# Optimization experiments

Measured on AMD Instinct MI355X. Metric: run time of the kernel, lower is better.

Reference implementation:

```python
import jax, jax.numpy as jnp
import numpy as np

B, L, D, H = 2, 1000, 288, 8
DIM = D // H          # 36 per-head dim
DFF = 2 * D           # 576 conv-FFN hidden
KS = L // 4           # 250 sampled keys per query
NQ = L // 4           # 250 selected (active) queries
EPS = 1e-5


def _layernorm(x, g, b):
    mu = x.mean(-1, keepdims=True)
    var = ((x - mu) ** 2).mean(-1, keepdims=True)
    return (x - mu) * jax.lax.rsqrt(var + EPS) * g + b


def _prob_attention(q, k, v, index_key):
    # q,k,v: [b,h,L,dim]; index_key: [L, KS]
    b, h, l, dim = q.shape
    # sample KS keys per query row (gather): [b,h,L,KS,dim]
    k_samp = jnp.take(k, index_key, axis=2)
    # sampled scores: [b,h,L,KS]
    scores_samp = jnp.einsum('bhld,bhlkd->bhlk', q, k_samp)
    # sparsity measure M(q) = max - mean(over full l_key, as in source)
    measure = scores_samp.max(-1) - scores_samp.sum(-1) / l
    # top-NQ active queries per (b,h): [b,h,NQ]
    idx_q = jax.lax.top_k(measure, NQ)[1]
    q_sel = jnp.take_along_axis(q, idx_q[..., None], axis=2)  # [b,h,NQ,dim]
    sim = jnp.einsum('bhqd,bhkd->bhqk', q_sel, k) * (1.0 / np.sqrt(dim))
    attn = jax.nn.softmax(sim, axis=-1)
    out_sel = jnp.einsum('bhqk,bhkd->bhqd', attn, v)          # [b,h,NQ,dim]
    # lazy queries get mean(V); scatter active outputs in
    out = jnp.broadcast_to(v.mean(axis=2, keepdims=True), v.shape)
    bi = jnp.arange(b)[:, None, None]
    hi = jnp.arange(h)[None, :, None]
    out = out.at[bi, hi, idx_q].set(out_sel)
    return out  # [b,h,L,dim]


def reference(x, index_key, Wq, bq, Wk, bk, Wv, bv, W1, b1, W2, b2,
              ln1_g, ln1_b, ln2_g, ln2_b):
    b, l, d = x.shape
    # QKV projections -> [b,h,L,dim]
    q = (x @ Wq.T + bq).reshape(b, l, H, DIM).transpose(0, 2, 1, 3)
    k = (x @ Wk.T + bk).reshape(b, l, H, DIM).transpose(0, 2, 1, 3)
    v = (x @ Wv.T + bv).reshape(b, l, H, DIM).transpose(0, 2, 1, 3)
    attn = _prob_attention(q, k, v, index_key)
    attn = attn.transpose(0, 2, 1, 3).reshape(b, l, d)
    # residual + LN1 (dropout is identity in eval)
    h1 = _layernorm(x + attn, ln1_g, ln1_b)
    # conv FFN (kernel_size=1 conv == per-position linear), exact GELU
    f = jax.nn.gelu(h1 @ W1.T + b1, approximate=False)   # [b,l,DFF]
    f = jax.nn.gelu(f @ W2.T + b2, approximate=False)    # [b,l,d]
    return _layernorm(f + h1, ln2_g, ln2_b)


def setup_inputs() -> dict:
    key = jax.random.key(0)
    ks = jax.random.split(key, 10)
    s = 0.05
    return {
        'x': jax.random.normal(ks[0], (B, L, D), jnp.float32),
        'index_key': jax.random.randint(ks[1], (L, KS), 0, L),
        'Wq': jax.random.normal(ks[2], (D, D), jnp.float32) * s,
        'bq': jnp.zeros((D,), jnp.float32),
        'Wk': jax.random.normal(ks[3], (D, D), jnp.float32) * s,
        'bk': jnp.zeros((D,), jnp.float32),
        'Wv': jax.random.normal(ks[4], (D, D), jnp.float32) * s,
        'bv': jnp.zeros((D,), jnp.float32),
        'W1': jax.random.normal(ks[5], (DFF, D), jnp.float32) * s,
        'b1': jnp.zeros((DFF,), jnp.float32),
        'W2': jax.random.normal(ks[6], (D, DFF), jnp.float32) * s,
        'b2': jnp.zeros((D,), jnp.float32),
        'ln1_g': jnp.ones((D,), jnp.float32),
        'ln1_b': jnp.zeros((D,), jnp.float32),
        'ln2_g': jnp.ones((D,), jnp.float32),
        'ln2_b': jnp.zeros((D,), jnp.float32),
    }
```

## Files before the change

kernel.cpp:

```cpp
#include <hip/hip_runtime.h>
#include <hip/hip_bf16.h>
#include <math.h>

#define B_ 2
#define L_ 1000
#define D_ 288
#define H_ 8
#define DIM_ 36
#define DFF_ 576
#define KS_ 250
#define NQ_ 250
#define BH_ (B_ * H_)
#define EPS_ 1e-5f
#define PSTRIDE_ 40

__device__ __forceinline__ float gelu_exact(float x) {
    return 0.5f * x * (1.0f + erff(x * 0.70710678118654752f));
}

__device__ __forceinline__ float dot4(float4 a, float4 b) {
    return a.x * b.x + a.y * b.y + a.z * b.z + a.w * b.w;
}

__global__ __launch_bounds__(256) void transpose_kernel(
    const float* __restrict__ src, float* __restrict__ dst,
    int Rr, int Cc, int ntx)
{
    __shared__ float tile[32][33];
    const int t = blockIdx.x;
    const int ty0 = (t / ntx) * 32, tx0 = (t % ntx) * 32;
    const int tx = threadIdx.x & 31, ty = threadIdx.x >> 5;
#pragma unroll
    for (int i = 0; i < 4; i++)
        tile[ty + 8 * i][tx] = src[(size_t)(ty0 + ty + 8 * i) * Cc + tx0 + tx];
    __syncthreads();
#pragma unroll
    for (int i = 0; i < 4; i++)
        dst[(size_t)(tx0 + ty + 8 * i) * Rr + ty0 + tx] = tile[tx][ty + 8 * i];
}

__global__ __launch_bounds__(256) void qkv_transpose_kernel(
    const float* __restrict__ Wq, const float* __restrict__ Wk,
    const float* __restrict__ Wv,
    float* __restrict__ WqT, float* __restrict__ WkT, float* __restrict__ WvT)
{
    __shared__ float tile[32][33];
    const int m = blockIdx.x / 81;
    const int t = blockIdx.x % 81;
    const float* src = (m == 0) ? Wq : (m == 1) ? Wk : Wv;
    float* dst = (m == 0) ? WqT : (m == 1) ? WkT : WvT;
    const int ty0 = (t / 9) * 32, tx0 = (t % 9) * 32;
    const int tx = threadIdx.x & 31, ty = threadIdx.x >> 5;
#pragma unroll
    for (int i = 0; i < 4; i++)
        tile[ty + 8 * i][tx] = src[(size_t)(ty0 + ty + 8 * i) * D_ + tx0 + tx];
    __syncthreads();
#pragma unroll
    for (int i = 0; i < 4; i++)
        dst[(size_t)(tx0 + ty + 8 * i) * D_ + ty0 + tx] = tile[tx][ty + 8 * i];
}

__global__ __launch_bounds__(256) void ktranspose_kernel(
    const float* __restrict__ K, float* __restrict__ KT)
{
    __shared__ float tile[32][33];
    const int t = blockIdx.x;
    const int bh = t >> 6;
    const int rem = t & 63;
    const int lt = rem >> 1, dt = rem & 1;
    const int l0 = lt * 32, d0 = dt * 32;
    const int tx = threadIdx.x & 31, ty = threadIdx.x >> 5;
    const float* Kb = K + (size_t)bh * L_ * DIM_;
    float* KTb = KT + (size_t)bh * DIM_ * L_;
#pragma unroll
    for (int i = 0; i < 4; i++) {
        int l = l0 + ty + 8 * i, d = d0 + tx;
        tile[ty + 8 * i][tx] = (l < L_ && d < DIM_) ? Kb[(size_t)l * DIM_ + d] : 0.f;
    }
    __syncthreads();
#pragma unroll
    for (int i = 0; i < 4; i++) {
        int d = d0 + ty + 8 * i, l = l0 + tx;
        if (d < DIM_ && l < L_) KTb[(size_t)d * L_ + l] = tile[tx][ty + 8 * i];
    }
}

__global__ __launch_bounds__(256) void qkvT2_kernel(
    const float* __restrict__ x,
    const float* __restrict__ WqT, const float* __restrict__ WkT,
    const float* __restrict__ WvT,
    const float* __restrict__ bq, const float* __restrict__ bk,
    const float* __restrict__ bv,
    float* __restrict__ Q, float* __restrict__ K, float* __restrict__ V)
{
    __shared__ float xsT[D_][4];
    const int base = blockIdx.x * 4;
    const int tid = threadIdx.x;

    for (int idx = tid; idx < 4 * D_; idx += 256) {
        int r = idx / D_, k = idx % D_;
        xsT[k][r] = x[(size_t)(base + r) * D_ + k];
    }
    __syncthreads();

    if (tid < 216) {
        const int gcol = 4 * tid;
        const int m = gcol / D_;
        const int c = gcol - m * D_;
        const float* WT = (m == 0) ? WqT : (m == 1) ? WkT : WvT;
        const float* bias = (m == 0) ? bq : (m == 1) ? bk : bv;
        float* outp = (m == 0) ? Q : (m == 1) ? K : V;

        float a[4][4];
#pragma unroll
        for (int j = 0; j < 4; j++) {
            float bv2 = bias[c + j];
#pragma unroll
            for (int r = 0; r < 4; r++) a[j][r] = bv2;
        }

        for (int k = 0; k < D_; k++) {
            float4 w = *(const float4*)(WT + (size_t)k * D_ + c);
            float4 xv = *(const float4*)&xsT[k][0];
            a[0][0] += w.x * xv.x; a[0][1] += w.x * xv.y; a[0][2] += w.x * xv.z; a[0][3] += w.x * xv.w;
            a[1][0] += w.y * xv.x; a[1][1] += w.y * xv.y; a[1][2] += w.y * xv.z; a[1][3] += w.y * xv.w;
            a[2][0] += w.z * xv.x; a[2][1] += w.z * xv.y; a[2][2] += w.z * xv.z; a[2][3] += w.z * xv.w;
            a[3][0] += w.w * xv.x; a[3][1] += w.w * xv.y; a[3][2] += w.w * xv.z; a[3][3] += w.w * xv.w;
        }

#pragma unroll
        for (int j = 0; j < 4; j++) {
            int col = c + j;
            int h = col / DIM_, dd = col % DIM_;
#pragma unroll
            for (int r = 0; r < 4; r++) {
                int row = base + r;
                int b = row / L_, l = row % L_;
                outp[((size_t)(b * H_ + h) * L_ + l) * DIM_ + dd] = a[j][r];
            }
        }
    }
}

__global__ __launch_bounds__(320) void qkv_kernel(
    const float* __restrict__ x,
    const float* __restrict__ Wq, const float* __restrict__ bq,
    const float* __restrict__ Wk, const float* __restrict__ bk,
    const float* __restrict__ Wv, const float* __restrict__ bv,
    float* __restrict__ Q, float* __restrict__ K, float* __restrict__ V)
{
    constexpr int R = 8;
    __shared__ float xs[R][D_];
    const int base = blockIdx.x * R;
    const int tid = threadIdx.x;

    const float4* xsrc = (const float4*)(x + (size_t)base * D_);
    float4* xdst = (float4*)&xs[0][0];
    for (int i = tid; i < R * D_ / 4; i += 320) xdst[i] = xsrc[i];
    __syncthreads();

    if (tid < D_) {
        const float4* wq4 = (const float4*)(Wq + (size_t)tid * D_);
        const float4* wk4 = (const float4*)(Wk + (size_t)tid * D_);
        const float4* wv4 = (const float4*)(Wv + (size_t)tid * D_);
        float aq[R], ak[R], av[R];
        float biasq = bq[tid], biask = bk[tid], biasv = bv[tid];
#pragma unroll
        for (int r = 0; r < R; r++) { aq[r] = biasq; ak[r] = biask; av[r] = biasv; }
        for (int d4 = 0; d4 < D_ / 4; d4++) {
            float4 wqv = wq4[d4], wkv = wk4[d4], wvv = wv4[d4];
#pragma unroll
            for (int r = 0; r < R; r++) {
                float4 hv = *(const float4*)&xs[r][d4 * 4];
                aq[r] += dot4(hv, wqv);
                ak[r] += dot4(hv, wkv);
                av[r] += dot4(hv, wvv);
            }
        }
        const int h = tid / DIM_, dd = tid % DIM_;
#pragma unroll
        for (int r = 0; r < R; r++) {
            int row = base + r;
            int b = row / L_, l = row % L_;
            size_t o = ((size_t)(b * H_ + h) * L_ + l) * DIM_ + dd;
            Q[o] = aq[r]; K[o] = ak[r]; V[o] = av[r];
        }
    }
}

__global__ __launch_bounds__(256) void vmean_kernel(
    const float* __restrict__ V, float* __restrict__ Vmean)
{
    const int bh = blockIdx.x;
    const int tid = threadIdx.x;
    __shared__ float red[7][DIM_];
    if (tid < 252) {
        int g = tid / DIM_, d = tid % DIM_;
        const float* base = V + (size_t)bh * L_ * DIM_;
        float s = 0.f;
        for (int l = g; l < L_; l += 7) s += base[l * DIM_ + d];
        red[g][d] = s;
    }
    __syncthreads();
    if (tid < DIM_) {
        float s = 0.f;
#pragma unroll
        for (int g = 0; g < 7; g++) s += red[g][tid];
        Vmean[bh * DIM_ + tid] = s * (1.0f / L_);
    }
}

__global__ __launch_bounds__(256) void score_measure3_kernel(
    const float* __restrict__ Q, const float* __restrict__ KT,
    const int* __restrict__ index_key, float* __restrict__ measure)
{
    constexpr int R = 8;
    __shared__ float qs[R][DIM_];
    __shared__ float st[R][1004];
    const int bh = blockIdx.x / 125;
    const int qt = blockIdx.x % 125;
    const int tid = threadIdx.x;

    if (tid < R * DIM_ / 4)
        ((float4*)&qs[0][0])[tid] =
            ((const float4*)(Q + ((size_t)bh * L_ + qt * R) * DIM_))[tid];
    __syncthreads();

    const float* KTb = KT + (size_t)bh * DIM_ * L_;
#pragma unroll
    for (int i = 0; i < 4; i++) {
        const int k = i * 256 + tid;
        if (k < L_) {
            float acc[R];
#pragma unroll
            for (int r = 0; r < R; r++) acc[r] = 0.f;
#pragma unroll
            for (int d4 = 0; d4 < DIM_ / 4; d4++) {
                float4 kv;
                kv.x = KTb[(size_t)(d4 * 4 + 0) * L_ + k];
                kv.y = KTb[(size_t)(d4 * 4 + 1) * L_ + k];
                kv.z = KTb[(size_t)(d4 * 4 + 2) * L_ + k];
                kv.w = KTb[(size_t)(d4 * 4 + 3) * L_ + k];
#pragma unroll
                for (int r = 0; r < R; r++)
                    acc[r] += dot4(*(const float4*)&qs[r][d4 * 4], kv);
            }
#pragma unroll
            for (int r = 0; r < R; r++) st[r][k] = acc[r];
        }
    }
    __syncthreads();

    const int r = tid >> 5;
    const int lane = tid & 31;
    const int l = qt * R + r;
    const int* ik = index_key + l * KS_;
    float mx = -1e30f, sm = 0.f;
    for (int s = lane; s < KS_; s += 32) {
        float v = st[r][ik[s]];
        mx = fmaxf(mx, v);
        sm += v;
    }
#pragma unroll
    for (int off = 16; off; off >>= 1) {
        mx = fmaxf(mx, __shfl_xor(mx, off));
        sm += __shfl_xor(sm, off);
    }
    if (lane == 0) measure[bh * L_ + l] = mx - sm * (1.0f / (float)L_);
}

__global__ __launch_bounds__(256) void measure_kernel(
    const float* __restrict__ Q, const float* __restrict__ K,
    const int* __restrict__ index_key, float* __restrict__ measure)
{
    const int w = threadIdx.x >> 6;
    const int lane = threadIdx.x & 63;
    const int wid = blockIdx.x * 4 + w;
    const int bh = wid / L_;
    const int l = wid % L_;

    const float4* qp = (const float4*)(Q + ((size_t)bh * L_ + l) * DIM_);
    float4 q[9];
#pragma unroll
    for (int i = 0; i < 9; i++) q[i] = qp[i];

    const int* ik = index_key + l * KS_;
    const float* Kb = K + (size_t)bh * L_ * DIM_;

    float mx = -1e30f, sm = 0.f;
#pragma unroll
    for (int s = lane; s < KS_; s += 64) {
        int kidx = ik[s];
        const float4* k4 = (const float4*)(Kb + (size_t)kidx * DIM_);
        float acc = 0.f;
#pragma unroll
        for (int i = 0; i < 9; i++) acc += dot4(q[i], k4[i]);
        mx = fmaxf(mx, acc);
        sm += acc;
    }
#pragma unroll
    for (int off = 32; off; off >>= 1) {
        mx = fmaxf(mx, __shfl_xor(mx, off));
        sm += __shfl_xor(sm, off);
    }
    if (lane == 0) measure[wid] = mx - sm * (1.0f / (float)L_);
}

__global__ __launch_bounds__(256) void topk_kernel(
    const float* __restrict__ measure, int* __restrict__ qlist,
    int* __restrict__ qcnt)
{
    const int bh = blockIdx.x >> 2;
    const int quarter = blockIdx.x & 3;
    __shared__ float m[L_];
    for (int i = threadIdx.x; i < L_; i += 256) m[i] = measure[bh * L_ + i];
    __syncthreads();
    const int i = quarter * 250 + threadIdx.x;
    if (threadIdx.x < 250) {
        float mi = m[i];
        int rank = 0;
        for (int j = 0; j < L_; j++) {
            float mj = m[j];
            rank += (mj > mi) || (mj == mi && j < i);
        }
        if (rank < NQ_) {
            int pos = atomicAdd(&qcnt[bh], 1);
            qlist[bh * NQ_ + pos] = i;
        }
    }
}

__global__ __launch_bounds__(256) void fill_kernel(
    const float* __restrict__ Vmean, float* __restrict__ attn_out)
{
    int idx = blockIdx.x * blockDim.x + threadIdx.x;
    if (idx >= B_ * L_ * D_) return;
    int d = idx % D_;
    int bl = idx / D_;
    int b = bl / L_;
    int h = d / DIM_, dd = d % DIM_;
    attn_out[idx] = Vmean[(b * H_ + h) * DIM_ + dd];
}

__global__ __launch_bounds__(256) void attn_part_kernel(
    const float* __restrict__ Q, const float* __restrict__ K,
    const float* __restrict__ V, const int* __restrict__ qlist,
    float* __restrict__ part, int nchunk, int chunk_len)
{
    const int bh = blockIdx.x / nchunk;
    const int chunk = blockIdx.x % nchunk;
    const int slot = threadIdx.x;
    if (slot >= NQ_) return;

    const int qidx = qlist[bh * NQ_ + slot];
    const float4* qp = (const float4*)(Q + ((size_t)bh * L_ + qidx) * DIM_);
    float4 q[9];
#pragma unroll
    for (int i = 0; i < 9; i++) q[i] = qp[i];

    const float* Kb = K + (size_t)bh * L_ * DIM_;
    const float* Vb = V + (size_t)bh * L_ * DIM_;
    const float scale = (float)(1.0 / 6.0);

    float4 acc[9];
#pragma unroll
    for (int i = 0; i < 9; i++) acc[i] = make_float4(0.f, 0.f, 0.f, 0.f);
    float sum = 0.f;

    const int k0 = chunk * chunk_len;
    for (int j = 0; j < chunk_len; j++) {
        const int key = k0 + j;
        const float4* kp = (const float4*)(Kb + (size_t)key * DIM_);
        float s = 0.f;
#pragma unroll
        for (int i = 0; i < 9; i++) s += dot4(q[i], kp[i]);
        float e = __expf(s * scale);
        sum += e;
        const float4* vp = (const float4*)(Vb + (size_t)key * DIM_);
#pragma unroll
        for (int i = 0; i < 9; i++) {
            float4 vv = vp[i];
            acc[i].x += e * vv.x;
            acc[i].y += e * vv.y;
            acc[i].z += e * vv.z;
            acc[i].w += e * vv.w;
        }
    }

    float* p = part + ((size_t)(bh * NQ_ + slot) * nchunk + chunk) * PSTRIDE_;
#pragma unroll
    for (int i = 0; i < 9; i++) ((float4*)p)[i] = acc[i];
    p[DIM_] = sum;
}

__global__ __launch_bounds__(256) void combine_kernel(
    const float* __restrict__ part, const int* __restrict__ qlist,
    float* __restrict__ attn_out, int nchunk)
{
    int idx = blockIdx.x * blockDim.x + threadIdx.x;
    if (idx >= BH_ * NQ_ * DIM_) return;
    int d = idx % DIM_;
    int bhslot = idx / DIM_;
    int bh = bhslot / NQ_, slot = bhslot % NQ_;
    const float* base = part + (size_t)bhslot * nchunk * PSTRIDE_;
    float a = 0.f, s = 0.f;
    for (int c = 0; c < nchunk; c++) {
        a += base[c * PSTRIDE_ + d];
        s += base[c * PSTRIDE_ + DIM_];
    }
    int qidx = qlist[bh * NQ_ + slot];
    int b = bh / H_, h = bh % H_;
    attn_out[((size_t)b * L_ + qidx) * D_ + h * DIM_ + d] = a / s;
}

__global__ __launch_bounds__(64) void ln1_kernel(
    const float* __restrict__ x, const float* __restrict__ attn,
    const float* __restrict__ g, const float* __restrict__ bb,
    float* __restrict__ h1)
{
    const int row = blockIdx.x;
    const int lane = threadIdx.x;
    const float* xr = x + (size_t)row * D_;
    const float* ar = attn + (size_t)row * D_;

    float vals[5];
    float s = 0.f;
#pragma unroll
    for (int i = 0; i < 5; i++) {
        int j = lane + i * 64;
        float v = (j < D_) ? (xr[j] + ar[j]) : 0.f;
        vals[i] = v;
        s += v;
    }
#pragma unroll
    for (int off = 32; off; off >>= 1) s += __shfl_xor(s, off);
    float mu = s * (1.0f / D_);

    float vs = 0.f;
#pragma unroll
    for (int i = 0; i < 5; i++) {
        int j = lane + i * 64;
        if (j < D_) { float dd = vals[i] - mu; vs += dd * dd; }
    }
#pragma unroll
    for (int off = 32; off; off >>= 1) vs += __shfl_xor(vs, off);
    float rstd = rsqrtf(vs * (1.0f / D_) + EPS_);

#pragma unroll
    for (int i = 0; i < 5; i++) {
        int j = lane + i * 64;
        if (j < D_) h1[(size_t)row * D_ + j] = (vals[i] - mu) * rstd * g[j] + bb[j];
    }
}

__global__ __launch_bounds__(288) void ffn_fused2b_kernel(
    const float* __restrict__ h1,
    const float* __restrict__ W1T, const float* __restrict__ b1,
    const float* __restrict__ W2T, const float* __restrict__ b2,
    const float* __restrict__ g, const float* __restrict__ bb,
    float* __restrict__ out)
{
    __shared__ float hs[4][D_];
    __shared__ float fs[4][DFF_];
    __shared__ float red[3456];
    __shared__ float ys[4][D_];
    const int base = blockIdx.x * 4;
    const int tid = threadIdx.x;

    {
        const float4* src = (const float4*)(h1 + (size_t)base * D_);
        float4* dst = (float4*)&hs[0][0];
        for (int i = tid; i < 4 * D_ / 4; i += 288) dst[i] = src[i];
    }
    __syncthreads();

    {
        const int kg = tid / 144;
        const int ct = tid - kg * 144;
        const int c = 4 * ct;
        float a[4][4];
        if (kg == 0) {
#pragma unroll
            for (int j = 0; j < 4; j++) {
                float bv = b1[c + j];
#pragma unroll
                for (int r = 0; r < 4; r++) a[j][r] = bv;
            }
        } else {
#pragma unroll
            for (int j = 0; j < 4; j++)
#pragma unroll
                for (int r = 0; r < 4; r++) a[j][r] = 0.f;
        }
        const int kbeg = kg * 144;
        for (int k = kbeg; k < kbeg + 144; k++) {
            float4 w = *(const float4*)(W1T + (size_t)k * DFF_ + c);
            float x0 = hs[0][k], x1 = hs[1][k], x2 = hs[2][k], x3 = hs[3][k];
            a[0][0] += w.x * x0; a[0][1] += w.x * x1; a[0][2] += w.x * x2; a[0][3] += w.x * x3;
            a[1][0] += w.y * x0; a[1][1] += w.y * x1; a[1][2] += w.y * x2; a[1][3] += w.y * x3;
            a[2][0] += w.z * x0; a[2][1] += w.z * x1; a[2][2] += w.z * x2; a[2][3] += w.z * x3;
            a[3][0] += w.w * x0; a[3][1] += w.w * x1; a[3][2] += w.w * x2; a[3][3] += w.w * x3;
        }
        if (kg == 1) {
#pragma unroll
            for (int j = 0; j < 4; j++)
                *(float4*)&red[(j * 144 + ct) * 4] =
                    make_float4(a[j][0], a[j][1], a[j][2], a[j][3]);
        }
        __syncthreads();
        if (kg == 0) {
            float y[4][4];
#pragma unroll
            for (int j = 0; j < 4; j++) {
                float4 o = *(const float4*)&red[(j * 144 + ct) * 4];
                y[j][0] = gelu_exact(a[j][0] + o.x);
                y[j][1] = gelu_exact(a[j][1] + o.y);
                y[j][2] = gelu_exact(a[j][2] + o.z);
                y[j][3] = gelu_exact(a[j][3] + o.w);
            }
#pragma unroll
            for (int r = 0; r < 4; r++)
                *(float4*)&fs[r][c] = make_float4(y[0][r], y[1][r], y[2][r], y[3][r]);
        }
    }
    __syncthreads();

    {
        const int kg = tid / 72;
        const int ct = tid - kg * 72;
        const int c = 4 * ct;
        float a[4][4];
        if (kg == 0) {
#pragma unroll
            for (int j = 0; j < 4; j++) {
                float bv = b2[c + j];
#pragma unroll
                for (int r = 0; r < 4; r++) a[j][r] = bv;
            }
        } else {
#pragma unroll
            for (int j = 0; j < 4; j++)
#pragma unroll
                for (int r = 0; r < 4; r++) a[j][r] = 0.f;
        }
        const int kbeg = kg * 144;
        for (int k = kbeg; k < kbeg + 144; k++) {
            float4 w = *(const float4*)(W2T + (size_t)k * D_ + c);
            float f0 = fs[0][k], f1 = fs[1][k], f2 = fs[2][k], f3 = fs[3][k];
            a[0][0] += w.x * f0; a[0][1] += w.x * f1; a[0][2] += w.x * f2; a[0][3] += w.x * f3;
            a[1][0] += w.y * f0; a[1][1] += w.y * f1; a[1][2] += w.y * f2; a[1][3] += w.y * f3;
            a[2][0] += w.z * f0; a[2][1] += w.z * f1; a[2][2] += w.z * f2; a[2][3] += w.z * f3;
            a[3][0] += w.w * f0; a[3][1] += w.w * f1; a[3][2] += w.w * f2; a[3][3] += w.w * f3;
        }
        if (kg >= 1) {
#pragma unroll
            for (int j = 0; j < 4; j++)
                *(float4*)&red[(((kg - 1) * 4 + j) * 72 + ct) * 4] =
                    make_float4(a[j][0], a[j][1], a[j][2], a[j][3]);
        }
        __syncthreads();
        if (kg == 0) {
            float y[4][4];
#pragma unroll
            for (int j = 0; j < 4; j++) {
                float4 o0 = *(const float4*)&red[((0 * 4 + j) * 72 + ct) * 4];
                float4 o1 = *(const float4*)&red[((1 * 4 + j) * 72 + ct) * 4];
                float4 o2 = *(const float4*)&red[((2 * 4 + j) * 72 + ct) * 4];
                y[j][0] = gelu_exact(a[j][0] + o0.x + o1.x + o2.x) + hs[0][c + j];
                y[j][1] = gelu_exact(a[j][1] + o0.y + o1.y + o2.y) + hs[1][c + j];
                y[j][2] = gelu_exact(a[j][2] + o0.z + o1.z + o2.z) + hs[2][c + j];
                y[j][3] = gelu_exact(a[j][3] + o0.w + o1.w + o2.w) + hs[3][c + j];
            }
#pragma unroll
            for (int r = 0; r < 4; r++)
                *(float4*)&ys[r][c] = make_float4(y[0][r], y[1][r], y[2][r], y[3][r]);
        }
    }
    __syncthreads();

    const int w = tid >> 6;
    const int lane = tid & 63;
    if (w < 4) {
        const int r = w;
        float s = 0.f, ss = 0.f;
#pragma unroll
        for (int i = 0; i < 5; i++) {
            int j = lane + i * 64;
            if (j < D_) { float y = ys[r][j]; s += y; ss += y * y; }
        }
#pragma unroll
        for (int off = 32; off; off >>= 1) {
            s += __shfl_xor(s, off);
            ss += __shfl_xor(ss, off);
        }
        float mu = s * (1.0f / D_);
        float var = ss * (1.0f / D_) - mu * mu;
        float rstd = rsqrtf(var + EPS_);
        int row = base + r;
#pragma unroll
        for (int i = 0; i < 5; i++) {
            int j = lane + i * 64;
            if (j < D_) out[(size_t)row * D_ + j] = (ys[r][j] - mu) * rstd * g[j] + bb[j];
        }
    }
}

__global__ __launch_bounds__(192) void ffn1_kernel(
    const float* __restrict__ h1,
    const float* __restrict__ W1, const float* __restrict__ b1,
    float* __restrict__ f1)
{
    constexpr int R = 8;
    __shared__ float hs[R][D_];
    const int base = blockIdx.x * R;
    const int tid = threadIdx.x;

    const float4* hsrc = (const float4*)(h1 + (size_t)base * D_);
    float4* hdst = (float4*)&hs[0][0];
    for (int i = tid; i < R * D_ / 4; i += 192) hdst[i] = hsrc[i];
    __syncthreads();

    const int j0 = tid, j1 = tid + 192, j2 = tid + 384;
    const float4* w0 = (const float4*)(W1 + (size_t)j0 * D_);
    const float4* w1 = (const float4*)(W1 + (size_t)j1 * D_);
    const float4* w2 = (const float4*)(W1 + (size_t)j2 * D_);
    float a0[R], a1[R], a2[R];
    float bb0 = b1[j0], bb1 = b1[j1], bb2 = b1[j2];
#pragma unroll
    for (int r = 0; r < R; r++) { a0[r] = bb0; a1[r] = bb1; a2[r] = bb2; }

    for (int d4 = 0; d4 < D_ / 4; d4++) {
        float4 x0 = w0[d4], x1 = w1[d4], x2 = w2[d4];
#pragma unroll
        for (int r = 0; r < R; r++) {
            float4 hv = *(const float4*)&hs[r][d4 * 4];
            a0[r] += dot4(hv, x0);
            a1[r] += dot4(hv, x1);
            a2[r] += dot4(hv, x2);
        }
    }
#pragma unroll
    for (int r = 0; r < R; r++) {
        size_t rowo = (size_t)(base + r) * DFF_;
        f1[rowo + j0] = gelu_exact(a0[r]);
        f1[rowo + j1] = gelu_exact(a1[r]);
        f1[rowo + j2] = gelu_exact(a2[r]);
    }
}

__global__ __launch_bounds__(320) void ffn2_ln_kernel(
    const float* __restrict__ f1, const float* __restrict__ h1,
    const float* __restrict__ W2, const float* __restrict__ b2,
    const float* __restrict__ g, const float* __restrict__ bb,
    float* __restrict__ out)
{
    constexpr int R = 8;
    __shared__ float fs[R][DFF_];
    __shared__ float hs[R][D_];
    __shared__ float ys[R][D_];
    const int base = blockIdx.x * R;
    const int tid = threadIdx.x;

    const float4* fsrc = (const float4*)(f1 + (size_t)base * DFF_);
    float4* fdst = (float4*)&fs[0][0];
    for (int i = tid; i < R * DFF_ / 4; i += 320) fdst[i] = fsrc[i];
    const float4* hsrc = (const float4*)(h1 + (size_t)base * D_);
    float4* hdst = (float4*)&hs[0][0];
    for (int i = tid; i < R * D_ / 4; i += 320) hdst[i] = hsrc[i];
    __syncthreads();

    if (tid < D_) {
        const float4* w4 = (const float4*)(W2 + (size_t)tid * DFF_);
        float acc[R];
        float bias = b2[tid];
#pragma unroll
        for (int r = 0; r < R; r++) acc[r] = bias;
        for (int d4 = 0; d4 < DFF_ / 4; d4++) {
            float4 wv = w4[d4];
#pragma unroll
            for (int r = 0; r < R; r++) {
                float4 fv = *(const float4*)&fs[r][d4 * 4];
                acc[r] += dot4(fv, wv);
            }
        }
#pragma unroll
        for (int r = 0; r < R; r++) ys[r][tid] = gelu_exact(acc[r]) + hs[r][tid];
    }
    __syncthreads();

    const int w = tid >> 6;
    const int lane = tid & 63;
    for (int r = w; r < R; r += 5) {
        float s = 0.f, ss = 0.f;
#pragma unroll
        for (int i = 0; i < 5; i++) {
            int j = lane + i * 64;
            if (j < D_) { float y = ys[r][j]; s += y; ss += y * y; }
        }
#pragma unroll
        for (int off = 32; off; off >>= 1) {
            s += __shfl_xor(s, off);
            ss += __shfl_xor(ss, off);
        }
        float mu = s * (1.0f / D_);
        float var = ss * (1.0f / D_) - mu * mu;
        float rstd = rsqrtf(var + EPS_);
        int row = base + r;
#pragma unroll
        for (int i = 0; i < 5; i++) {
            int j = lane + i * 64;
            if (j < D_) out[(size_t)row * D_ + j] = (ys[r][j] - mu) * rstd * g[j] + bb[j];
        }
    }
}

extern "C" void kernel_launch(void* const* d_in, const int* in_sizes, int n_in,
                              void* d_out, int out_size, void* d_ws, size_t ws_size,
                              hipStream_t stream)
{
    const float* x         = (const float*)d_in[0];
    const int*   index_key = (const int*)  d_in[1];
    const float* Wq = (const float*)d_in[2];
    const float* bq = (const float*)d_in[3];
    const float* Wk = (const float*)d_in[4];
    const float* bk = (const float*)d_in[5];
    const float* Wv = (const float*)d_in[6];
    const float* bv = (const float*)d_in[7];
    const float* W1 = (const float*)d_in[8];
    const float* b1 = (const float*)d_in[9];
    const float* W2 = (const float*)d_in[10];
    const float* b2 = (const float*)d_in[11];
    const float* ln1_g = (const float*)d_in[12];
    const float* ln1_b = (const float*)d_in[13];
    const float* ln2_g = (const float*)d_in[14];
    const float* ln2_b = (const float*)d_in[15];
    float* out = (float*)d_out;

    float* Q        = (float*)d_ws;
    float* K        = Q + 576000;
    float* V        = K + 576000;
    float* Vmean    = V + 576000;
    float* measure  = Vmean + 576;
    float* attn_out = measure + 16000;
    float* h1       = attn_out + 576000;
    int*   qlist    = (int*)(h1 + 576000);
    int*   qcnt     = qlist + 4000;
    float* part     = (float*)(qcnt + 16);
    float* f1       = part;
    float* KT       = part + 4000000;

    float* WqT = part;
    float* WkT = WqT + 82944;
    float* WvT = WkT + 82944;
    float* W1T = part;
    float* W2T = part + 165888;

    const size_t kt_end = 2900592ull + 4000000ull + 576000ull;
    const bool   big    = ws_size >= kt_end * sizeof(float);
    const int    nchunk = big ? 25 : 8;
    const int    chunk_len = L_ / nchunk;

    if (big) {
        qkv_transpose_kernel<<<243, 256, 0, stream>>>(Wq, Wk, Wv, WqT, WkT, WvT);
        qkvT2_kernel<<<500, 256, 0, stream>>>(x, WqT, WkT, WvT, bq, bk, bv, Q, K, V);
    } else {
        qkv_kernel<<<250, 320, 0, stream>>>(x, Wq, bq, Wk, bk, Wv, bv, Q, K, V);
    }
    vmean_kernel<<<BH_, 256, 0, stream>>>(V, Vmean);
    if (big) {
        ktranspose_kernel<<<BH_ * 64, 256, 0, stream>>>(K, KT);
        score_measure3_kernel<<<BH_ * 125, 256, 0, stream>>>(Q, KT, index_key, measure);
    } else {
        measure_kernel<<<4000, 256, 0, stream>>>(Q, K, index_key, measure);
    }
    hipMemsetAsync(qcnt, 0, BH_ * sizeof(int), stream);
    topk_kernel<<<BH_ * 4, 256, 0, stream>>>(measure, qlist, qcnt);
    fill_kernel<<<(B_ * L_ * D_ + 255) / 256, 256, 0, stream>>>(Vmean, attn_out);
    attn_part_kernel<<<BH_ * nchunk, 256, 0, stream>>>(Q, K, V, qlist, part, nchunk, chunk_len);
    combine_kernel<<<(BH_ * NQ_ * DIM_ + 255) / 256, 256, 0, stream>>>(part, qlist, attn_out, nchunk);
    ln1_kernel<<<B_ * L_, 64, 0, stream>>>(x, attn_out, ln1_g, ln1_b, h1);
    if (big) {
        transpose_kernel<<<162, 256, 0, stream>>>(W1, W1T, DFF_, D_, 9);
        transpose_kernel<<<162, 256, 0, stream>>>(W2, W2T, D_, DFF_, 18);
        ffn_fused2b_kernel<<<500, 288, 0, stream>>>(h1, W1T, b1, W2T, b2, ln2_g, ln2_b, out);
    } else {
        ffn1_kernel<<<250, 192, 0, stream>>>(h1, W1, b1, f1);
        ffn2_ln_kernel<<<250, 320, 0, stream>>>(f1, h1, W2, b2, ln2_g, ln2_b, out);
    }
}
```

Before: 309.5 us.

## Merge topk/fill/combine via slot map and fuse FFN weight transposes

```diff
diff --git a/kernel.cpp b/kernel.cpp
--- a/kernel.cpp
+++ b/kernel.cpp
@@ -22,23 +22,6 @@
     return a.x * b.x + a.y * b.y + a.z * b.z + a.w * b.w;
 }
 
-__global__ __launch_bounds__(256) void transpose_kernel(
-    const float* __restrict__ src, float* __restrict__ dst,
-    int Rr, int Cc, int ntx)
-{
-    __shared__ float tile[32][33];
-    const int t = blockIdx.x;
-    const int ty0 = (t / ntx) * 32, tx0 = (t % ntx) * 32;
-    const int tx = threadIdx.x & 31, ty = threadIdx.x >> 5;
-#pragma unroll
-    for (int i = 0; i < 4; i++)
-        tile[ty + 8 * i][tx] = src[(size_t)(ty0 + ty + 8 * i) * Cc + tx0 + tx];
-    __syncthreads();
-#pragma unroll
-    for (int i = 0; i < 4; i++)
-        dst[(size_t)(tx0 + ty + 8 * i) * Rr + ty0 + tx] = tile[tx][ty + 8 * i];
-}
-
 __global__ __launch_bounds__(256) void qkv_transpose_kernel(
     const float* __restrict__ Wq, const float* __restrict__ Wk,
     const float* __restrict__ Wv,
@@ -58,6 +41,26 @@
 #pragma unroll
     for (int i = 0; i < 4; i++)
         dst[(size_t)(tx0 + ty + 8 * i) * D_ + ty0 + tx] = tile[tx][ty + 8 * i];
+}
+
+__global__ __launch_bounds__(256) void ffn_transpose_kernel(
+    const float* __restrict__ W1, const float* __restrict__ W2,
+    float* __restrict__ W1T, float* __restrict__ W2T)
+{
+    __shared__ float tile[32][33];
+    int t = blockIdx.x;
+    const float* src; float* dst; int Rr, Cc, ntx;
+    if (t < 162) { src = W1; dst = W1T; Rr = DFF_; Cc = D_; ntx = 9; }
+    else { t -= 162; src = W2; dst = W2T; Rr = D_; Cc = DFF_; ntx = 18; }
+    const int ty0 = (t / ntx) * 32, tx0 = (t % ntx) * 32;
+    const int tx = threadIdx.x & 31, ty = threadIdx.x >> 5;
+#pragma unroll
+    for (int i = 0; i < 4; i++)
+        tile[ty + 8 * i][tx] = src[(size_t)(ty0 + ty + 8 * i) * Cc + tx0 + tx];
+    __syncthreads();
+#pragma unroll
+    for (int i = 0; i < 4; i++)
+        dst[(size_t)(tx0 + ty + 8 * i) * Rr + ty0 + tx] = tile[tx][ty + 8 * i];
 }
 
 __global__ __launch_bounds__(256) void ktranspose_kernel(
@@ -306,40 +309,25 @@
     if (lane == 0) measure[wid] = mx - sm * (1.0f / (float)L_);
 }
 
-__global__ __launch_bounds__(256) void topk_kernel(
+__global__ __launch_bounds__(1024) void topk2_kernel(
     const float* __restrict__ measure, int* __restrict__ qlist,
-    int* __restrict__ qcnt)
-{
-    const int bh = blockIdx.x >> 2;
-    const int quarter = blockIdx.x & 3;
+    int* __restrict__ slot_map)
+{
+    const int bh = blockIdx.x;
     __shared__ float m[L_];
-    for (int i = threadIdx.x; i < L_; i += 256) m[i] = measure[bh * L_ + i];
-    __syncthreads();
-    const int i = quarter * 250 + threadIdx.x;
-    if (threadIdx.x < 250) {
-        float mi = m[i];
+    const int tid = threadIdx.x;
+    for (int i = tid; i < L_; i += 1024) m[i] = measure[bh * L_ + i];
+    __syncthreads();
+    if (tid < L_) {
+        float mi = m[tid];
         int rank = 0;
         for (int j = 0; j < L_; j++) {
             float mj = m[j];
-            rank += (mj > mi) || (mj == mi && j < i);
-        }
-        if (rank < NQ_) {
-            int pos = atomicAdd(&qcnt[bh], 1);
-            qlist[bh * NQ_ + pos] = i;
-        }
-    }
-}
-
-__global__ __launch_bounds__(256) void fill_kernel(
-    const float* __restrict__ Vmean, float* __restrict__ attn_out)
-{
-    int idx = blockIdx.x * blockDim.x + threadIdx.x;
-    if (idx >= B_ * L_ * D_) return;
-    int d = idx % D_;
-    int bl = idx / D_;
-    int b = bl / L_;
-    int h = d / DIM_, dd = d % DIM_;
-    attn_out[idx] = Vmean[(b * H_ + h) * DIM_ + dd];
+            rank += (mj > mi) || (mj == mi && j < tid);
+        }
+        if (rank < NQ_) qlist[bh * NQ_ + rank] = tid;
+        slot_map[bh * L_ + tid] = (rank < NQ_) ? rank : -1;
+    }
 }
 
 __global__ __launch_bounds__(256) void attn_part_kernel(
@@ -393,24 +381,31 @@
     p[DIM_] = sum;
 }
 
-__global__ __launch_bounds__(256) void combine_kernel(
-    const float* __restrict__ part, const int* __restrict__ qlist,
-    float* __restrict__ attn_out, int nchunk)
+__global__ __launch_bounds__(256) void combine_all_kernel(
+    const float* __restrict__ part, const int* __restrict__ slot_map,
+    const float* __restrict__ Vmean, float* __restrict__ attn_out, int nchunk)
 {
     int idx = blockIdx.x * blockDim.x + threadIdx.x;
-    if (idx >= BH_ * NQ_ * DIM_) return;
-    int d = idx % DIM_;
-    int bhslot = idx / DIM_;
-    int bh = bhslot / NQ_, slot = bhslot % NQ_;
-    const float* base = part + (size_t)bhslot * nchunk * PSTRIDE_;
-    float a = 0.f, s = 0.f;
-    for (int c = 0; c < nchunk; c++) {
-        a += base[c * PSTRIDE_ + d];
-        s += base[c * PSTRIDE_ + DIM_];
-    }
-    int qidx = qlist[bh * NQ_ + slot];
-    int b = bh / H_, h = bh % H_;
-    attn_out[((size_t)b * L_ + qidx) * D_ + h * DIM_ + d] = a / s;
+    if (idx >= B_ * L_ * D_) return;
+    int dfull = idx % D_;
+    int bl = idx / D_;
+    int b = bl / L_, l = bl % L_;
+    int h = dfull / DIM_, d = dfull % DIM_;
+    int bh = b * H_ + h;
+    int slot = slot_map[bh * L_ + l];
+    float v;
+    if (slot < 0) {
+        v = Vmean[bh * DIM_ + d];
+    } else {
+        const float* p = part + (size_t)(bh * NQ_ + slot) * nchunk * PSTRIDE_;
+        float a = 0.f, s = 0.f;
+        for (int c = 0; c < nchunk; c++) {
+            a += p[c * PSTRIDE_ + d];
+            s += p[c * PSTRIDE_ + DIM_];
+        }
+        v = a / s;
+    }
+    attn_out[idx] = v;
 }
 
 __global__ __launch_bounds__(64) void ln1_kernel(
@@ -744,8 +739,8 @@
     float* attn_out = measure + 16000;
     float* h1       = attn_out + 576000;
     int*   qlist    = (int*)(h1 + 576000);
-    int*   qcnt     = qlist + 4000;
-    float* part     = (float*)(qcnt + 16);
+    int*   slot_map = qlist + 4000;
+    float* part     = (float*)(slot_map + 16000);
     float* f1       = part;
     float* KT       = part + 4000000;
 
@@ -755,7 +750,7 @@
     float* W1T = part;
     float* W2T = part + 165888;
 
-    const size_t kt_end = 2900592ull + 4000000ull + 576000ull;
+    const size_t kt_end = 2916576ull + 4000000ull + 576000ull;
     const bool   big    = ws_size >= kt_end * sizeof(float);
     const int    nchunk = big ? 25 : 8;
     const int    chunk_len = L_ / nchunk;
@@ -773,15 +768,13 @@
     } else {
         measure_kernel<<<4000, 256, 0, stream>>>(Q, K, index_key, measure);
     }
-    hipMemsetAsync(qcnt, 0, BH_ * sizeof(int), stream);
-    topk_kernel<<<BH_ * 4, 256, 0, stream>>>(measure, qlist, qcnt);
-    fill_kernel<<<(B_ * L_ * D_ + 255) / 256, 256, 0, stream>>>(Vmean, attn_out);
+    topk2_kernel<<<BH_, 1024, 0, stream>>>(measure, qlist, slot_map);
     attn_part_kernel<<<BH_ * nchunk, 256, 0, stream>>>(Q, K, V, qlist, part, nchunk, chunk_len);
-    combine_kernel<<<(BH_ * NQ_ * DIM_ + 255) / 256, 256, 0, stream>>>(part, qlist, attn_out, nchunk);
+    combine_all_kernel<<<(B_ * L_ * D_ + 255) / 256, 256, 0, stream>>>(
+        part, slot_map, Vmean, attn_out, nchunk);
     ln1_kernel<<<B_ * L_, 64, 0, stream>>>(x, attn_out, ln1_g, ln1_b, h1);
     if (big) {
-        transpose_kernel<<<162, 256, 0, stream>>>(W1, W1T, DFF_, D_, 9);
-        transpose_kernel<<<162, 256, 0, stream>>>(W2, W2T, D_, DFF_, 18);
+        ffn_transpose_kernel<<<324, 256, 0, stream>>>(W1, W2, W1T, W2T);
         ffn_fused2b_kernel<<<500, 288, 0, stream>>>(h1, W1T, b1, W2T, b2, ln2_g, ln2_b, out);
     } else {
         ffn1_kernel<<<250, 192, 0, stream>>>(h1, W1, b1, f1);
```

Result: no change. 313.4 us (+1.3%).
